# Optimization experiments

Hardware: AMD Instinct MI355X
Metric: run time of the kernel (lower is better)

Reference implementation:

```python
import jax, jax.numpy as jnp
import numpy as np

NUM_HEADS = 16
HEAD_DIM = 128
HIDDEN = NUM_HEADS * HEAD_DIM


def rotate_half(x):
    x1, x2 = jnp.split(x, 2, axis=-1)
    return jnp.concatenate((-x2, x1), axis=-1)


def setup_inputs() -> dict:
    key = jax.random.key(0)
    ks = jax.random.split(key, 7)
    b, s = 2, 2048
    return {
        "hidden_states": jax.random.normal(ks[0], (b, s, HIDDEN), dtype=jnp.float32),
        "cos": jax.random.normal(ks[1], (1, 1, s, HEAD_DIM), dtype=jnp.float32),
        "sin": jax.random.normal(ks[2], (1, 1, s, HEAD_DIM), dtype=jnp.float32),
        "Wq": jax.random.normal(ks[3], (HIDDEN, HIDDEN), dtype=jnp.float32) * 0.02,
        "Wk": jax.random.normal(ks[4], (HIDDEN, HIDDEN), dtype=jnp.float32) * 0.02,
        "Wv": jax.random.normal(ks[5], (HIDDEN, HIDDEN), dtype=jnp.float32) * 0.02,
        "Wo": jax.random.normal(ks[6], (HIDDEN, HIDDEN), dtype=jnp.float32) * 0.02,
    }


def reference(hidden_states, cos, sin, Wq, Wk, Wv, Wo):
    b, s, _ = hidden_states.shape

    def proj(W):
        # [b,s,hidden] -> [b,H,s,D]
        return (hidden_states @ W).reshape(b, s, NUM_HEADS, HEAD_DIM).transpose(0, 2, 1, 3)

    q = proj(Wq)
    k = proj(Wk)
    v = proj(Wv)

    # RoPE: cos/sin [1,1,s,D] broadcast over batch and heads
    q = q * cos + rotate_half(q) * sin
    k = k * cos + rotate_half(k) * sin

    scale = 1.0 / jnp.sqrt(jnp.asarray(HEAD_DIM, dtype=q.dtype))
    scores = jnp.einsum("bhqd,bhkd->bhqk", q, k) * scale  # [b,H,s,s]
    attn = jax.nn.softmax(scores, axis=-1)  # no mask applied (matches source)
    out = jnp.einsum("bhqk,bhkd->bhqd", attn, v)  # [b,H,s,D]
    out = out.transpose(0, 2, 1, 3).reshape(b, s, HIDDEN)
    return out @ Wo
```

## Files before the change

### kernel.cpp

```cpp
#include <hip/hip_runtime.h>

typedef short bf16x8 __attribute__((ext_vector_type(8)));
typedef float f32x4 __attribute__((ext_vector_type(4)));

#define HID   2048
#define S_LEN 2048
#define NH    16
#define HD    128
#define BATCH 2
#define NROWS (BATCH * S_LEN)

__device__ __forceinline__ float bf2f(unsigned short u) {
    union { unsigned int i; float f; } v;
    v.i = ((unsigned int)u) << 16;
    return v.f;
}
__device__ __forceinline__ unsigned short f2bf(float f) {
    union { float f; unsigned int i; } v;
    v.f = f;
    unsigned int u = v.i;
    return (unsigned short)((u + 0x7fffu + ((u >> 16) & 1u)) >> 16);
}

__device__ __forceinline__ unsigned int pkbf(float a, float b) {
#if defined(__has_builtin) && __has_builtin(__builtin_amdgcn_cvt_pk_bf16_f32)
    typedef __bf16 bf2_t __attribute__((ext_vector_type(2)));
    bf2_t v = __builtin_amdgcn_cvt_pk_bf16_f32(a, b);
    unsigned int u;
    __builtin_memcpy(&u, &v, 4);
    return u;
#else
    return (unsigned int)f2bf(a) | ((unsigned int)f2bf(b) << 16);
#endif
}

__device__ __forceinline__ float exp2_fast(float x) {
#if defined(__has_builtin) && __has_builtin(__builtin_amdgcn_exp2f)
    return __builtin_amdgcn_exp2f(x);
#else
    return __expf(x * 0.6931471805599453f);
#endif
}

__device__ __forceinline__ void async16(const unsigned short* g, unsigned short* l) {
    __builtin_amdgcn_global_load_lds(
        (const __attribute__((address_space(1))) unsigned int*)g,
        (__attribute__((address_space(3))) unsigned int*)l, 16, 0, 0);
}

__global__ __launch_bounds__(256) void prep(const float* __restrict__ hs,
                                            const float* __restrict__ Wa,
                                            const float* __restrict__ Wb,
                                            const float* __restrict__ Wc,
                                            unsigned short* __restrict__ Xb,
                                            unsigned short* __restrict__ WT) {
    int z = blockIdx.z;
    int t = threadIdx.x;
    if (z >= 3) {
        size_t blk = (size_t)(z - 3) * 2048 + blockIdx.y * 64 + blockIdx.x;
        size_t idx = (blk * 256 + t) * 8;
        float4 v0 = *(const float4*)(hs + idx);
        float4 v1 = *(const float4*)(hs + idx + 4);
        uint4 o;
        o.x = pkbf(v0.x, v0.y);
        o.y = pkbf(v0.z, v0.w);
        o.z = pkbf(v1.x, v1.y);
        o.w = pkbf(v1.z, v1.w);
        *(uint4*)(Xb + idx) = o;
        return;
    }
    __shared__ float tile[64][33];
    int tx = t & 31, ty = t >> 5;
    int bx = blockIdx.x, by = blockIdx.y;
    const float* W = (z == 0) ? Wa : ((z == 1) ? Wb : Wc);
    unsigned short* dst = WT + (size_t)z * HID * HID;
#pragma unroll
    for (int i = 0; i < 8; i++)
        tile[ty + i * 8][tx] = W[(size_t)(by * 64 + ty + i * 8) * HID + bx * 32 + tx];
    __syncthreads();
    int k2 = tx * 2;
#pragma unroll
    for (int i = 0; i < 4; i++) {
        int j = ty + i * 8;
        *(unsigned int*)(dst + (size_t)(bx * 32 + j) * HID + by * 64 + k2) =
            pkbf(tile[k2][j], tile[k2 + 1][j]);
    }
}

__global__ __launch_bounds__(256) void transpose_cast(const float* __restrict__ W,
                                                      unsigned short* __restrict__ WT) {
    __shared__ float tile[64][33];
    int t = threadIdx.x;
    int tx = t & 31, ty = t >> 5;
    int bx = blockIdx.x, by = blockIdx.y;
#pragma unroll
    for (int i = 0; i < 8; i++)
        tile[ty + i * 8][tx] = W[(size_t)(by * 64 + ty + i * 8) * HID + bx * 32 + tx];
    __syncthreads();
    int k2 = tx * 2;
#pragma unroll
    for (int i = 0; i < 4; i++) {
        int j = ty + i * 8;
        *(unsigned int*)(WT + (size_t)(bx * 32 + j) * HID + by * 64 + k2) =
            pkbf(tile[k2][j], tile[k2 + 1][j]);
    }
}

template <int MODE>
__global__ __launch_bounds__(256, 2) void gemm_bt(const unsigned short* __restrict__ A,
                                                  const unsigned short* __restrict__ Bt,
                                                  unsigned short* __restrict__ Qo,
                                                  unsigned short* __restrict__ Ko,
                                                  unsigned short* __restrict__ Vo,
                                                  float* __restrict__ Fo,
                                                  const float* __restrict__ cosp,
                                                  const float* __restrict__ sinp,
                                                  int n_shift) {
    __shared__ unsigned short SM[16384];
    unsigned short* Asm = SM;
    unsigned short* Bsm = SM + 8192;
    int t = threadIdx.x;
    int wave = t >> 6, lane = t & 63;
    int wm = wave >> 1, wn = wave & 1;
    int c = lane & 15, quad = lane >> 4;
    int m0 = blockIdx.y * 128, nloc = blockIdx.x * 128;

    int lr = lane >> 3;
    int cb = (lane & 7) ^ (lr & 7);
    const unsigned short* Ag = A + (size_t)(m0 + wave * 32 + lr) * HID + cb * 8;
    const unsigned short* Bg = Bt + (size_t)(nloc + wave * 32 + lr) * HID + cb * 8;
    unsigned short* Al = Asm + wave * 2048;
    unsigned short* Bl = Bsm + wave * 2048;

    f32x4 zero = {0.f, 0.f, 0.f, 0.f};
    f32x4 acc[4][4];
#pragma unroll
    for (int i = 0; i < 4; i++)
#pragma unroll
        for (int j = 0; j < 4; j++) acc[i][j] = zero;

    for (int it = 0; it < 32; it++) {
        int k0 = it * 64;
#pragma unroll
        for (int j = 0; j < 4; j++) {
            async16(Ag + k0 + j * 8 * HID, Al + j * 512);
            async16(Bg + k0 + j * 8 * HID, Bl + j * 512);
        }
        __syncthreads();
#pragma unroll
        for (int kk = 0; kk < 2; kk++) {
            bf16x8 af[4], bfr[4];
#pragma unroll
            for (int mt = 0; mt < 4; mt++)
                af[mt] = *(const bf16x8*)(Asm + (wm * 64 + mt * 16 + c) * 64 +
                                          (((kk * 4 + quad) ^ (c & 7)) * 8));
#pragma unroll
            for (int nt = 0; nt < 4; nt++)
                bfr[nt] = *(const bf16x8*)(Bsm + (wn * 64 + nt * 16 + c) * 64 +
                                           (((kk * 4 + quad) ^ (c & 7)) * 8));
#pragma unroll
            for (int mt = 0; mt < 4; mt++)
#pragma unroll
                for (int nt = 0; nt < 4; nt++)
                    acc[mt][nt] = __builtin_amdgcn_mfma_f32_16x16x32_bf16(af[mt], bfr[nt],
                                                                          acc[mt][nt], 0, 0, 0);
        }
        __syncthreads();
    }

    if (MODE == 2) {
#pragma unroll
        for (int mt = 0; mt < 4; mt++)
#pragma unroll
            for (int nt = 0; nt < 4; nt++)
#pragma unroll
                for (int r = 0; r < 4; r++) {
                    int row = m0 + wm * 64 + mt * 16 + quad * 4 + r;
                    int col = nloc + wn * 64 + nt * 16 + c;
                    Fo[(size_t)row * HID + col] = acc[mt][nt][r];
                }
    } else {
        int nglob0 = n_shift + nloc;
        int mat = nglob0 >> 11;
        int h = (nglob0 & 2047) >> 7;
        if (mat == 2) {
#pragma unroll
            for (int mt = 0; mt < 4; mt++)
#pragma unroll
                for (int nt = 0; nt < 4; nt++) {
                    int d = wn * 64 + nt * 16 + c;
                    int row0 = m0 + wm * 64 + mt * 16 + quad * 4;
                    int b = row0 >> 11, s = row0 & 2047;
                    ushort4 o;
                    o.x = f2bf(acc[mt][nt][0]);
                    o.y = f2bf(acc[mt][nt][1]);
                    o.z = f2bf(acc[mt][nt][2]);
                    o.w = f2bf(acc[mt][nt][3]);
                    *(ushort4*)(Vo + ((size_t)(b * NH + h) * HD + d) * S_LEN + s) = o;
                }
        } else {
            unsigned short* Cb = (mat == 0) ? Qo : Ko;
            float scl = (mat == 0) ? 0.12751743f : 1.0f;
            __syncthreads();
#pragma unroll
            for (int mt = 0; mt < 4; mt++)
#pragma unroll
                for (int nt = 0; nt < 4; nt++) {
                    ushort4 o;
                    o.x = f2bf(acc[mt][nt][0]);
                    o.y = f2bf(acc[mt][nt][1]);
                    o.z = f2bf(acc[mt][nt][2]);
                    o.w = f2bf(acc[mt][nt][3]);
                    *(ushort4*)(SM + (mt * 4 + nt) * 1024 + t * 4) = o;
                }
            __syncthreads();
            int partner = (wm * 2 + (wn ^ 1)) * 64 + lane;
            float sgn = wn ? 1.0f : -1.0f;
#pragma unroll
            for (int mt = 0; mt < 4; mt++) {
#pragma unroll
                for (int nt = 0; nt < 4; nt++) {
                    ushort4 pv = *(const ushort4*)(SM + (mt * 4 + nt) * 1024 + partner * 4);
                    float part[4] = {bf2f(pv.x), bf2f(pv.y), bf2f(pv.z), bf2f(pv.w)};
                    int col = wn * 64 + nt * 16 + c;
#pragma unroll
                    for (int r = 0; r < 4; r++) {
                        int row = m0 + wm * 64 + mt * 16 + quad * 4 + r;
                        int b = row >> 11, s = row & 2047;
                        float cv = cosp[s * HD + col], sv = sinp[s * HD + col];
                        float out = (acc[mt][nt][r] * cv + sgn * part[r] * sv) * scl;
                        Cb[((size_t)(b * NH + h) * S_LEN + s) * HD + col] = f2bf(out);
                    }
                }
            }
        }
    }
}

#define PKS 72
__global__ __launch_bounds__(256, 2) void attn_kernel(const unsigned short* __restrict__ Q,
                                                      const unsigned short* __restrict__ Kg,
                                                      const unsigned short* __restrict__ Vt,
                                                      unsigned short* __restrict__ Aout) {
    __shared__ unsigned short Ksm[2 * 64 * 128];
    __shared__ unsigned short Vsm[128 * 64];
    __shared__ __align__(16) unsigned short Psm[4 * 2 * 16 * PKS];
    int bh = blockIdx.y;
    int b = bh >> 4, h = bh & 15;
    int t = threadIdx.x;
    int wave = t >> 6, lane = t & 63;
    int c = lane & 15, quad = lane >> 4;
    int q0 = blockIdx.x * 128 + wave * 32;
    const unsigned short* Qp = Q + (size_t)bh * S_LEN * HD;
    const unsigned short* Kp = Kg + (size_t)bh * S_LEN * HD;
    const unsigned short* Vp = Vt + (size_t)bh * HD * S_LEN;

    bf16x8 qf[2][4];
#pragma unroll
    for (int qn = 0; qn < 2; qn++)
#pragma unroll
        for (int kk = 0; kk < 4; kk++)
            qf[qn][kk] = *(const bf16x8*)(Qp + (size_t)(q0 + qn * 16 + c) * HD + kk * 32 + quad * 8);

    f32x4 zero = {0.f, 0.f, 0.f, 0.f};
    f32x4 o_acc[2][8];
#pragma unroll
    for (int qn = 0; qn < 2; qn++)
#pragma unroll
        for (int nt = 0; nt < 8; nt++) o_acc[qn][nt] = zero;
    float lsum[2] = {0.f, 0.f};

#define STAGE_K(CH, BUF) {                                                      \
    _Pragma("unroll")                                                           \
    for (int j = 0; j < 4; j++) {                                               \
        int fc = (wave * 4 + j) * 64 + lane;                                    \
        int rK = fc >> 4, cbK = (fc & 15) ^ (rK & 15);                          \
        async16(Kp + (size_t)((CH) * 64 + rK) * HD + cbK * 8,                   \
                Ksm + (BUF) * 8192 + (wave * 4 + j) * 512); } }
#define STAGE_V(CH) {                                                           \
    _Pragma("unroll")                                                           \
    for (int j = 0; j < 4; j++) {                                               \
        int fc = (wave * 4 + j) * 64 + lane;                                    \
        int rV = fc >> 3, cbV = (fc & 7) ^ (rV & 7);                            \
        async16(Vp + (size_t)rV * S_LEN + (CH) * 64 + cbV * 8,                  \
                Vsm + (wave * 4 + j) * 512); } }

    STAGE_K(0, 0);
    STAGE_V(0);
    STAGE_K(1, 1);

    for (int i = 0; i < 32; i++) {
        const unsigned short* Kb = Ksm + (i & 1) * 8192;
        __builtin_amdgcn_s_waitcnt(0x0F78);
        __builtin_amdgcn_s_barrier();
        __builtin_amdgcn_sched_barrier(0);

        f32x4 sacc[4][2];
#pragma unroll
        for (int km = 0; km < 4; km++)
#pragma unroll
            for (int qn = 0; qn < 2; qn++) sacc[km][qn] = zero;
        __builtin_amdgcn_s_setprio(1);
#pragma unroll
        for (int kk = 0; kk < 4; kk++) {
            bf16x8 kfr[4];
#pragma unroll
            for (int km = 0; km < 4; km++)
                kfr[km] = *(const bf16x8*)(Kb + (km * 16 + c) * HD + (((kk * 4 + quad) ^ c)) * 8);
#pragma unroll
            for (int km = 0; km < 4; km++)
#pragma unroll
                for (int qn = 0; qn < 2; qn++)
                    sacc[km][qn] = __builtin_amdgcn_mfma_f32_16x16x32_bf16(kfr[km], qf[qn][kk],
                                                                           sacc[km][qn], 0, 0, 0);
        }
        __builtin_amdgcn_s_setprio(0);

#pragma unroll
        for (int qn = 0; qn < 2; qn++) {
#pragma unroll
            for (int km = 0; km < 4; km++) {
                float e0 = exp2_fast(sacc[km][qn][0]);
                float e1 = exp2_fast(sacc[km][qn][1]);
                float e2 = exp2_fast(sacc[km][qn][2]);
                float e3 = exp2_fast(sacc[km][qn][3]);
                lsum[qn] += (e0 + e1) + (e2 + e3);
                uint2 pk;
                pk.x = pkbf(e0, e1);
                pk.y = pkbf(e2, e3);
                *(uint2*)(Psm + ((wave * 2 + qn) * 16 + c) * PKS + km * 16 + quad * 4) = pk;
            }
        }
        asm volatile("" ::: "memory");
        __builtin_amdgcn_s_waitcnt(0xc07f);
        asm volatile("" ::: "memory");

        __builtin_amdgcn_sched_barrier(0);
        __builtin_amdgcn_s_waitcnt(0x0F74);
        __builtin_amdgcn_s_barrier();
        __builtin_amdgcn_sched_barrier(0);

        __builtin_amdgcn_s_setprio(1);
#pragma unroll
        for (int kf = 0; kf < 2; kf++) {
            bf16x8 pf[2];
#pragma unroll
            for (int qn = 0; qn < 2; qn++)
                pf[qn] = *(const bf16x8*)(Psm + ((wave * 2 + qn) * 16 + c) * PKS + kf * 32 + quad * 8);
#pragma unroll
            for (int nt = 0; nt < 8; nt++) {
                bf16x8 vf = *(const bf16x8*)(Vsm + (nt * 16 + c) * 64 +
                                             (((kf * 4 + quad) ^ (c & 7))) * 8);
#pragma unroll
                for (int qn = 0; qn < 2; qn++)
                    o_acc[qn][nt] = __builtin_amdgcn_mfma_f32_16x16x32_bf16(pf[qn], vf,
                                                                            o_acc[qn][nt], 0, 0, 0);
            }
        }
        __builtin_amdgcn_s_setprio(0);
        __builtin_amdgcn_sched_barrier(0);
        __builtin_amdgcn_s_barrier();
        __builtin_amdgcn_sched_barrier(0);

        int nv = (i + 1 > 31) ? 31 : i + 1;
        int nk = (i + 2 > 31) ? 31 : i + 2;
        STAGE_V(nv);
        STAGE_K(nk, (i & 1));
    }
#undef STAGE_K
#undef STAGE_V

#pragma unroll
    for (int qn = 0; qn < 2; qn++) {
        lsum[qn] += __shfl_xor(lsum[qn], 16);
        lsum[qn] += __shfl_xor(lsum[qn], 32);
    }
    float inv[2][4];
#pragma unroll
    for (int qn = 0; qn < 2; qn++)
#pragma unroll
        for (int r = 0; r < 4; r++)
            inv[qn][r] = 1.0f / __shfl(lsum[qn], quad * 4 + r);

#pragma unroll
    for (int qn = 0; qn < 2; qn++) {
#pragma unroll
        for (int r = 0; r < 4; r++) {
            int srow = q0 + qn * 16 + quad * 4 + r;
            size_t base = ((size_t)(b * S_LEN + srow)) * HID + h * HD;
#pragma unroll
            for (int nt = 0; nt < 8; nt++)
                Aout[base + nt * 16 + c] = f2bf(o_acc[qn][nt][r] * inv[qn][r]);
        }
    }
}

extern "C" void kernel_launch(void* const* d_in, const int* in_sizes, int n_in,
                              void* d_out, int out_size, void* d_ws, size_t ws_size,
                              hipStream_t stream) {
    const float* hs   = (const float*)d_in[0];
    const float* cosp = (const float*)d_in[1];
    const float* sinp = (const float*)d_in[2];
    const float* Wq   = (const float*)d_in[3];
    const float* Wk   = (const float*)d_in[4];
    const float* Wv   = (const float*)d_in[5];
    const float* Wo   = (const float*)d_in[6];

    char* ws = (char*)d_ws;
    unsigned short* Xb = (unsigned short*)(ws);
    unsigned short* Qb = (unsigned short*)(ws + (16ull << 20));
    unsigned short* Kb = (unsigned short*)(ws + (32ull << 20));
    unsigned short* Vb = (unsigned short*)(ws + (48ull << 20));
    unsigned short* WT = (unsigned short*)(ws + (64ull << 20));

    const bool fused = ws_size >= (88ull << 20);

    if (fused) {
        prep<<<dim3(64, 32, 5), 256, 0, stream>>>(hs, Wq, Wk, Wv, Xb, WT);
        gemm_bt<0><<<dim3(48, 32), 256, 0, stream>>>(Xb, WT, Qb, Kb, Vb, nullptr,
                                                     cosp, sinp, 0);
        attn_kernel<<<dim3(16, 32), 256, 0, stream>>>(Qb, Kb, Vb, Xb );
        unsigned short* WoT = (unsigned short*)(ws + (16ull << 20));
        transpose_cast<<<dim3(64, 32), 256, 0, stream>>>(Wo, WoT);
        gemm_bt<2><<<dim3(16, 32), 256, 0, stream>>>(Xb, WoT, nullptr, nullptr, nullptr,
                                                     (float*)d_out, cosp, sinp, 0);
    } else {
        prep<<<dim3(64, 32, 5), 256, 0, stream>>>(hs, Wq, Wq, Wq, Xb, WT);
        gemm_bt<0><<<dim3(16, 32), 256, 0, stream>>>(Xb, WT, Qb, Kb, Vb, nullptr,
                                                     cosp, sinp, 0);
        transpose_cast<<<dim3(64, 32), 256, 0, stream>>>(Wk, WT);
        gemm_bt<0><<<dim3(16, 32), 256, 0, stream>>>(Xb, WT, Qb, Kb, Vb, nullptr,
                                                     cosp, sinp, 2048);
        transpose_cast<<<dim3(64, 32), 256, 0, stream>>>(Wv, WT);
        gemm_bt<0><<<dim3(16, 32), 256, 0, stream>>>(Xb, WT, Qb, Kb, Vb, nullptr,
                                                     cosp, sinp, 4096);
        attn_kernel<<<dim3(16, 32), 256, 0, stream>>>(Qb, Kb, Vb, Xb );
        transpose_cast<<<dim3(64, 32), 256, 0, stream>>>(Wo, WT);
        gemm_bt<2><<<dim3(16, 32), 256, 0, stream>>>(Xb, WT, nullptr, nullptr, nullptr,
                                                     (float*)d_out, cosp, sinp, 0);
    }
}
```

Measured before the change: 388.5 us.

## Switch attention to 32x32x16 MFMA and keep P in registers via permlane32 swap

The attention kernel moves from 16x16x32 to 32x32x16 bf16 MFMA tiles for both QK^T and PV. The exponentiated scores are packed to bf16 and rearranged across half-waves with v_permlane32_swap, so they feed the PV MFMA directly from registers instead of round-tripping through the shared-memory P buffer. This removes the LDS writes and reads for P and the wait they required, and cuts the number of K/V fragment loads per MFMA. The risk is correctness of the lane mapping and higher register pressure from the 16-wide accumulators.

```diff
diff --git a/kernel.cpp b/kernel.cpp
--- a/kernel.cpp
+++ b/kernel.cpp
@@ -2,6 +2,7 @@
 
 typedef short bf16x8 __attribute__((ext_vector_type(8)));
 typedef float f32x4 __attribute__((ext_vector_type(4)));
+typedef float f32x16 __attribute__((ext_vector_type(16)));
 
 #define HID   2048
 #define S_LEN 2048
@@ -237,38 +238,33 @@
     }
 }
 
-#define PKS 72
 __global__ __launch_bounds__(256, 2) void attn_kernel(const unsigned short* __restrict__ Q,
                                                       const unsigned short* __restrict__ Kg,
                                                       const unsigned short* __restrict__ Vt,
                                                       unsigned short* __restrict__ Aout) {
     __shared__ unsigned short Ksm[2 * 64 * 128];
     __shared__ unsigned short Vsm[128 * 64];
-    __shared__ __align__(16) unsigned short Psm[4 * 2 * 16 * PKS];
     int bh = blockIdx.y;
     int b = bh >> 4, h = bh & 15;
     int t = threadIdx.x;
     int wave = t >> 6, lane = t & 63;
-    int c = lane & 15, quad = lane >> 4;
+    int w31 = lane & 31, hi = lane >> 5;
     int q0 = blockIdx.x * 128 + wave * 32;
     const unsigned short* Qp = Q + (size_t)bh * S_LEN * HD;
     const unsigned short* Kp = Kg + (size_t)bh * S_LEN * HD;
     const unsigned short* Vp = Vt + (size_t)bh * HD * S_LEN;
 
-    bf16x8 qf[2][4];
-#pragma unroll
-    for (int qn = 0; qn < 2; qn++)
-#pragma unroll
-        for (int kk = 0; kk < 4; kk++)
-            qf[qn][kk] = *(const bf16x8*)(Qp + (size_t)(q0 + qn * 16 + c) * HD + kk * 32 + quad * 8);
-
-    f32x4 zero = {0.f, 0.f, 0.f, 0.f};
-    f32x4 o_acc[2][8];
-#pragma unroll
-    for (int qn = 0; qn < 2; qn++)
-#pragma unroll
-        for (int nt = 0; nt < 8; nt++) o_acc[qn][nt] = zero;
-    float lsum[2] = {0.f, 0.f};
+    bf16x8 qf[8];
+#pragma unroll
+    for (int kb = 0; kb < 8; kb++)
+        qf[kb] = *(const bf16x8*)(Qp + (size_t)(q0 + w31) * HD + kb * 16 + hi * 8);
+
+    f32x16 o_acc[4];
+#pragma unroll
+    for (int dt = 0; dt < 4; dt++)
+#pragma unroll
+        for (int r = 0; r < 16; r++) o_acc[dt][r] = 0.f;
+    float lsum = 0.f;
 
 #define STAGE_K(CH, BUF) {                                                      \
     _Pragma("unroll")                                                           \
@@ -285,6 +281,21 @@
         async16(Vp + (size_t)rV * S_LEN + (CH) * 64 + cbV * 8,                  \
                 Vsm + (wave * 4 + j) * 512); } }
 
+#define SM_PACK(S, PA0, PA1) {                                                  \
+    float e_[16];                                                               \
+    _Pragma("unroll")                                                           \
+    for (int r_ = 0; r_ < 16; r_++) { e_[r_] = exp2_fast((S)[r_]); lsum += e_[r_]; } \
+    unsigned int a0_ = pkbf(e_[0], e_[1]),  b0_ = pkbf(e_[4], e_[5]);           \
+    unsigned int a1_ = pkbf(e_[2], e_[3]),  b1_ = pkbf(e_[6], e_[7]);           \
+    asm volatile("v_permlane32_swap_b32 %0, %1" : "+v"(a0_), "+v"(b0_));        \
+    asm volatile("v_permlane32_swap_b32 %0, %1" : "+v"(a1_), "+v"(b1_));        \
+    { uint4 w_ = {a0_, a1_, b0_, b1_}; __builtin_memcpy(&PA0, &w_, 16); }       \
+    unsigned int c0_ = pkbf(e_[8], e_[9]),   d0_ = pkbf(e_[12], e_[13]);        \
+    unsigned int c1_ = pkbf(e_[10], e_[11]), d1_ = pkbf(e_[14], e_[15]);        \
+    asm volatile("v_permlane32_swap_b32 %0, %1" : "+v"(c0_), "+v"(d0_));        \
+    asm volatile("v_permlane32_swap_b32 %0, %1" : "+v"(c1_), "+v"(d1_));        \
+    { uint4 w_ = {c0_, c1_, d0_, d1_}; __builtin_memcpy(&PA1, &w_, 16); } }
+
     STAGE_K(0, 0);
     STAGE_V(0);
     STAGE_K(1, 1);
@@ -295,45 +306,23 @@
         __builtin_amdgcn_s_barrier();
         __builtin_amdgcn_sched_barrier(0);
 
-        f32x4 sacc[4][2];
-#pragma unroll
-        for (int km = 0; km < 4; km++)
-#pragma unroll
-            for (int qn = 0; qn < 2; qn++) sacc[km][qn] = zero;
+        f32x16 s0, s1;
+#pragma unroll
+        for (int r = 0; r < 16; r++) { s0[r] = 0.f; s1[r] = 0.f; }
         __builtin_amdgcn_s_setprio(1);
 #pragma unroll
-        for (int kk = 0; kk < 4; kk++) {
-            bf16x8 kfr[4];
-#pragma unroll
-            for (int km = 0; km < 4; km++)
-                kfr[km] = *(const bf16x8*)(Kb + (km * 16 + c) * HD + (((kk * 4 + quad) ^ c)) * 8);
-#pragma unroll
-            for (int km = 0; km < 4; km++)
-#pragma unroll
-                for (int qn = 0; qn < 2; qn++)
-                    sacc[km][qn] = __builtin_amdgcn_mfma_f32_16x16x32_bf16(kfr[km], qf[qn][kk],
-                                                                           sacc[km][qn], 0, 0, 0);
+        for (int kb = 0; kb < 8; kb++) {
+            int ch = ((kb * 2 + hi) ^ (w31 & 15)) * 8;
+            bf16x8 k0 = *(const bf16x8*)(Kb + (size_t)w31 * 128 + ch);
+            bf16x8 k1 = *(const bf16x8*)(Kb + (size_t)(32 + w31) * 128 + ch);
+            s0 = __builtin_amdgcn_mfma_f32_32x32x16_bf16(k0, qf[kb], s0, 0, 0, 0);
+            s1 = __builtin_amdgcn_mfma_f32_32x32x16_bf16(k1, qf[kb], s1, 0, 0, 0);
         }
         __builtin_amdgcn_s_setprio(0);
 
-#pragma unroll
-        for (int qn = 0; qn < 2; qn++) {
-#pragma unroll
-            for (int km = 0; km < 4; km++) {
-                float e0 = exp2_fast(sacc[km][qn][0]);
-                float e1 = exp2_fast(sacc[km][qn][1]);
-                float e2 = exp2_fast(sacc[km][qn][2]);
-                float e3 = exp2_fast(sacc[km][qn][3]);
-                lsum[qn] += (e0 + e1) + (e2 + e3);
-                uint2 pk;
-                pk.x = pkbf(e0, e1);
-                pk.y = pkbf(e2, e3);
-                *(uint2*)(Psm + ((wave * 2 + qn) * 16 + c) * PKS + km * 16 + quad * 4) = pk;
-            }
-        }
-        asm volatile("" ::: "memory");
-        __builtin_amdgcn_s_waitcnt(0xc07f);
-        asm volatile("" ::: "memory");
+        bf16x8 pa[4];
+        SM_PACK(s0, pa[0], pa[1]);
+        SM_PACK(s1, pa[2], pa[3]);
 
         __builtin_amdgcn_sched_barrier(0);
         __builtin_amdgcn_s_waitcnt(0x0F74);
@@ -342,19 +331,13 @@
 
         __builtin_amdgcn_s_setprio(1);
 #pragma unroll
-        for (int kf = 0; kf < 2; kf++) {
-            bf16x8 pf[2];
-#pragma unroll
-            for (int qn = 0; qn < 2; qn++)
-                pf[qn] = *(const bf16x8*)(Psm + ((wave * 2 + qn) * 16 + c) * PKS + kf * 32 + quad * 8);
-#pragma unroll
-            for (int nt = 0; nt < 8; nt++) {
-                bf16x8 vf = *(const bf16x8*)(Vsm + (nt * 16 + c) * 64 +
-                                             (((kf * 4 + quad) ^ (c & 7))) * 8);
-#pragma unroll
-                for (int qn = 0; qn < 2; qn++)
-                    o_acc[qn][nt] = __builtin_amdgcn_mfma_f32_16x16x32_bf16(pf[qn], vf,
-                                                                            o_acc[qn][nt], 0, 0, 0);
+        for (int dt = 0; dt < 4; dt++) {
+#pragma unroll
+            for (int ks = 0; ks < 4; ks++) {
+                bf16x8 vf = *(const bf16x8*)(Vsm + (size_t)(dt * 32 + w31) * 64 +
+                                             (((ks * 2 + hi) ^ (w31 & 7)) * 8));
+                o_acc[dt] = __builtin_amdgcn_mfma_f32_32x32x16_bf16(pa[ks], vf,
+                                                                    o_acc[dt], 0, 0, 0);
             }
         }
         __builtin_amdgcn_s_setprio(0);
@@ -369,28 +352,22 @@
     }
 #undef STAGE_K
 #undef STAGE_V
-
-#pragma unroll
-    for (int qn = 0; qn < 2; qn++) {
-        lsum[qn] += __shfl_xor(lsum[qn], 16);
-        lsum[qn] += __shfl_xor(lsum[qn], 32);
-    }
-    float inv[2][4];
-#pragma unroll
-    for (int qn = 0; qn < 2; qn++)
-#pragma unroll
-        for (int r = 0; r < 4; r++)
-            inv[qn][r] = 1.0f / __shfl(lsum[qn], quad * 4 + r);
-
-#pragma unroll
-    for (int qn = 0; qn < 2; qn++) {
-#pragma unroll
-        for (int r = 0; r < 4; r++) {
-            int srow = q0 + qn * 16 + quad * 4 + r;
-            size_t base = ((size_t)(b * S_LEN + srow)) * HID + h * HD;
-#pragma unroll
-            for (int nt = 0; nt < 8; nt++)
-                Aout[base + nt * 16 + c] = f2bf(o_acc[qn][nt][r] * inv[qn][r]);
+#undef SM_PACK
+
+    lsum += __shfl_xor(lsum, 32);
+    float invv = 1.0f / lsum;
+    float inv[16];
+#pragma unroll
+    for (int r = 0; r < 16; r++)
+        inv[r] = __shfl(invv, (r & 3) + 8 * (r >> 2) + 4 * hi);
+
+#pragma unroll
+    for (int dt = 0; dt < 4; dt++) {
+#pragma unroll
+        for (int r = 0; r < 16; r++) {
+            int srow = q0 + (r & 3) + 8 * (r >> 2) + 4 * hi;
+            Aout[((size_t)(b * S_LEN + srow)) * HID + h * HD + dt * 32 + w31] =
+                f2bf(o_acc[dt][r] * inv[r]);
         }
     }
 }
```

Result: faster. 379.2 us (median of 2 runs) (-2.4%).
